# Kernel tuning notes

Measured on AMD Instinct MI355X. Metric: run time of the kernel, lower is better.

The kernel has to match this reference:

```python
import jax, jax.numpy as jnp
import numpy as np

N = 50000
E = 400000
F_IN = 128
HID = 64
HEADS = 4
OUT_HEADS = 4
N_CLS = 121
NEG_SLOPE = 0.2


def _gat_layer(x, src, dst, W, a_src, a_dst, b, heads, out_ch, concat):
    n = x.shape[0]
    xh = (x @ W).reshape(n, heads, out_ch)                      # [N,H,C]
    alpha_s = jnp.sum(xh * a_src, axis=-1)                      # [N,H]
    alpha_d = jnp.sum(xh * a_dst, axis=-1)                      # [N,H]
    logits = jax.nn.leaky_relu(alpha_s[src] + alpha_d[dst], NEG_SLOPE)  # [E,H]
    # numerically stable edge softmax per destination node
    m = jax.ops.segment_max(logits, dst, num_segments=n)        # [N,H]
    e = jnp.exp(logits - m[dst])                                # [E,H]
    denom = jax.ops.segment_sum(e, dst, num_segments=n)         # [N,H]
    alpha = e / (denom[dst] + 1e-16)                            # [E,H]
    msg = alpha[:, :, None] * xh[src]                           # [E,H,C]
    out = jax.ops.segment_sum(msg, dst, num_segments=n)         # [N,H,C]
    if concat:
        out = out.reshape(n, heads * out_ch)
    else:
        out = out.mean(axis=1)
    return out + b


def setup_inputs() -> dict:
    key = jax.random.key(0)
    ks = jax.random.split(key, 20)
    x = jax.random.normal(ks[0], (N, F_IN), dtype=jnp.float32)
    edge_index = jax.random.randint(ks[1], (2, E), 0, N, dtype=jnp.int32)
    s = lambda *sh: 1.0 / np.sqrt(sh[0])
    inp = {
        'x': x,
        'edge_index': edge_index,
        # conv1: F_IN -> HEADS*HID
        'W1': jax.random.normal(ks[2], (F_IN, HEADS * HID), jnp.float32) * s(F_IN),
        'a1_src': jax.random.normal(ks[3], (HEADS, HID), jnp.float32) * s(HID),
        'a1_dst': jax.random.normal(ks[4], (HEADS, HID), jnp.float32) * s(HID),
        'b1': jnp.zeros((HEADS * HID,), jnp.float32),
        'lin1_W': jax.random.normal(ks[5], (F_IN, HEADS * HID), jnp.float32) * s(F_IN),
        'lin1_b': jnp.zeros((HEADS * HID,), jnp.float32),
        # conv2: HEADS*HID -> HEADS*HID
        'W2': jax.random.normal(ks[6], (HEADS * HID, HEADS * HID), jnp.float32) * s(HEADS * HID),
        'a2_src': jax.random.normal(ks[7], (HEADS, HID), jnp.float32) * s(HID),
        'a2_dst': jax.random.normal(ks[8], (HEADS, HID), jnp.float32) * s(HID),
        'b2': jnp.zeros((HEADS * HID,), jnp.float32),
        # conv3: HEADS*HID -> N_CLS (mean over OUT_HEADS)
        'W3': jax.random.normal(ks[9], (HEADS * HID, OUT_HEADS * N_CLS), jnp.float32) * s(HEADS * HID),
        'a3_src': jax.random.normal(ks[10], (OUT_HEADS, N_CLS), jnp.float32) * s(N_CLS),
        'a3_dst': jax.random.normal(ks[11], (OUT_HEADS, N_CLS), jnp.float32) * s(N_CLS),
        'b3': jnp.zeros((N_CLS,), jnp.float32),
        'lin3_W': jax.random.normal(ks[12], (HEADS * HID, N_CLS), jnp.float32) * s(HEADS * HID),
        'lin3_b': jnp.zeros((N_CLS,), jnp.float32),
    }
    return inp


def reference(x, edge_index, W1, a1_src, a1_dst, b1, lin1_W, lin1_b,
              W2, a2_src, a2_dst, b2, W3, a3_src, a3_dst, b3, lin3_W, lin3_b):
    src, dst = edge_index[0], edge_index[1]
    h = _gat_layer(x, src, dst, W1, a1_src, a1_dst, b1, HEADS, HID, True) + (x @ lin1_W + lin1_b)
    h = jax.nn.elu(h)
    h = _gat_layer(h, src, dst, W2, a2_src, a2_dst, b2, HEADS, HID, True) + h  # residual skip (no lin2)
    h = jax.nn.elu(h)
    out = _gat_layer(h, src, dst, W3, a3_src, a3_dst, b3, OUT_HEADS, N_CLS, False) + (h @ lin3_W + lin3_b)
    return out
```

## Files before the change

### kernel.cpp

```cpp
#include <hip/hip_runtime.h>
#include <cstdint>
#include <cstddef>

#define F_IN 128
#define HC12 256
#define HC3 484
#define NCLS 121

typedef unsigned short u16;
typedef unsigned int u32;
typedef __attribute__((ext_vector_type(8))) short short8;
typedef __attribute__((ext_vector_type(8))) __fp16 half8;
typedef __attribute__((ext_vector_type(4))) float float4v;

static __device__ __forceinline__ float lrelu(float x) { return x > 0.f ? x : 0.2f * x; }

static __device__ __forceinline__ u16 f2h(float f) {
    union { __fp16 h; u16 u; } v; v.h = (__fp16)f; return v.u;
}
static __device__ __forceinline__ float h2f(u16 u) {
    union { u16 u; __fp16 h; } v; v.u = u; return (float)v.h;
}

static __device__ __forceinline__ void gload16(const u16* g, u16* l) {
    __builtin_amdgcn_global_load_lds((const __attribute__((address_space(1))) void*)g,
                                     (__attribute__((address_space(3))) void*)l,
                                     16, 0, 0);
}

__global__ void hist_kernel(const int* __restrict__ dst, int* __restrict__ deg, int E) {
    int e = blockIdx.x * 256 + threadIdx.x;
    if (e < E) atomicAdd(&deg[dst[e]], 1);
}

__global__ __launch_bounds__(1024) void scan_kernel(const int* __restrict__ deg,
                                                    int* __restrict__ rowp, int N) {
    __shared__ int swave[16];
    __shared__ int s_carry;
    int tid = threadIdx.x;
    int w = tid >> 6, lane = tid & 63;
    if (tid == 0) { rowp[0] = 0; s_carry = 0; }
    __syncthreads();
    for (int base = 0; base < N; base += 4096) {
        int i0 = base + tid * 4;
        int v0 = (i0     < N) ? deg[i0]     : 0;
        int v1 = (i0 + 1 < N) ? deg[i0 + 1] : 0;
        int v2 = (i0 + 2 < N) ? deg[i0 + 2] : 0;
        int v3 = (i0 + 3 < N) ? deg[i0 + 3] : 0;
        int t = v0 + v1 + v2 + v3;
        int sc = t;
#pragma unroll
        for (int off = 1; off < 64; off <<= 1) {
            int u = __shfl_up(sc, off, 64);
            if (lane >= off) sc += u;
        }
        if (lane == 63) swave[w] = sc;
        __syncthreads();
        if (w == 0) {
            int ws = (lane < 16) ? swave[lane] : 0;
#pragma unroll
            for (int off = 1; off < 16; off <<= 1) {
                int u = __shfl_up(ws, off, 64);
                if (lane >= off) ws += u;
            }
            if (lane < 16) swave[lane] = ws;
        }
        __syncthreads();
        int carry = s_carry;
        int tb = carry + ((w > 0) ? swave[w - 1] : 0) + sc - t;
        if (i0     < N) rowp[i0 + 1] = tb + v0;
        if (i0 + 1 < N) rowp[i0 + 2] = tb + v0 + v1;
        if (i0 + 2 < N) rowp[i0 + 3] = tb + v0 + v1 + v2;
        if (i0 + 3 < N) rowp[i0 + 4] = tb + t;
        __syncthreads();
        if (tid == 1023) s_carry = carry + swave[15];
        __syncthreads();
    }
}

__global__ void scatter_kernel(const int* __restrict__ src, const int* __restrict__ dst,
                               const int* __restrict__ rowp, int* __restrict__ cur,
                               int* __restrict__ col, int E) {
    int e = blockIdx.x * 256 + threadIdx.x;
    if (e < E) {
        int d = dst[e];
        int pos = rowp[d] + atomicAdd(&cur[d], 1);
        col[pos] = src[e];
    }
}

__global__ void cvtT_all_kernel(const float* W1, const float* l1W, const float* W2,
                                const float* W3, const float* l3W,
                                u16* C1, u16* C2, u16* C3) {
    int i = blockIdx.x * 256 + threadIdx.x;
    const float* B; u16* o; int K, N;
    if (i < 32768)       { B = W1;  o = C1;             K = 128; N = 256; }
    else if (i < 65536)  { B = l1W; o = C1 + 256 * 128; K = 128; N = 256; i -= 32768; }
    else if (i < 131072) { B = W2;  o = C2;             K = 256; N = 256; i -= 65536; }
    else if (i < 254976) { B = W3;  o = C3;             K = 256; N = 484; i -= 131072; }
    else if (i < 285952) { B = l3W; o = C3 + 484 * 256; K = 256; N = 121; i -= 254976; }
    else return;
    int n = i % N, k = i / N;
    o[(size_t)n * K + k] = f2h(B[(size_t)k * N + n]);
}

__global__ __launch_bounds__(256) void xcvt_kernel(const float* __restrict__ x,
                                                   u16* __restrict__ o, int total8) {
    int i = blockIdx.x * 256 + threadIdx.x;
    if (i >= total8) return;
    const float4* p = (const float4*)(x + (size_t)i * 8);
    float4 a = p[0], b = p[1];
    union { u16 u[8]; short8 v; } r;
    r.u[0] = f2h(a.x); r.u[1] = f2h(a.y); r.u[2] = f2h(a.z); r.u[3] = f2h(a.w);
    r.u[4] = f2h(b.x); r.u[5] = f2h(b.y); r.u[6] = f2h(b.z); r.u[7] = f2h(b.w);
    *(short8*)(o + (size_t)i * 8) = r.v;
}

#define BM 128
#define BN 128
#define BK 32

__global__ __launch_bounds__(256, 3) void gemm_f16(const u16* __restrict__ A16,
                                                   const u16* __restrict__ BT,
                                                   int M, int K, int Ntot,
                                                   int nx, int ny,
                                                   int Nb, u16* __restrict__ Cb, int strideB,
                                                   float* __restrict__ Cf,
                                                   const float* __restrict__ biasf, int strideF) {
    __shared__ __align__(16) u16 sA[BM * BK];
    __shared__ __align__(16) u16 sB[BN * BK];
    int tid = threadIdx.x;
    int wave = tid >> 6, lane = tid & 63;
    int wr = wave >> 1, wc = wave & 1;

    int bid = blockIdx.x;
    int G = nx * 8;
    int g = bid / G;
    int rem = ny - g * 8;
    int rb, cb;
    if (rem >= 8) {
        int r = bid - g * G;
        rb = g * 8 + (r & 7);
        cb = r >> 3;
    } else {
        int t = bid - g * G;
        rb = g * 8 + t % rem;
        cb = t / rem;
    }
    int m0 = rb * BM, n0 = cb * BN;

    int fm = lane & 15;
    int q = lane >> 4;

    int srow = lane >> 2;
    int sch = (lane & 3) * 8;
    u16* lA0 = &sA[(wave * 32) * BK];
    u16* lA1 = &sA[(wave * 32 + 16) * BK];
    u16* lB0 = &sB[(wave * 32) * BK];
    u16* lB1 = &sB[(wave * 32 + 16) * BK];
    int ar0 = min(m0 + wave * 32 + srow, M - 1);
    int ar1 = min(m0 + wave * 32 + 16 + srow, M - 1);
    int br0 = min(n0 + wave * 32 + srow, Ntot - 1);
    int br1 = min(n0 + wave * 32 + 16 + srow, Ntot - 1);

    float4v acc[4][4];
#pragma unroll
    for (int i = 0; i < 4; i++)
#pragma unroll
        for (int j = 0; j < 4; j++) acc[i][j] = (float4v){0.f, 0.f, 0.f, 0.f};

    for (int kc = 0; kc < K; kc += BK) {
        gload16(&A16[(size_t)ar0 * K + kc + sch], lA0);
        gload16(&A16[(size_t)ar1 * K + kc + sch], lA1);
        gload16(&BT[(size_t)br0 * K + kc + sch], lB0);
        gload16(&BT[(size_t)br1 * K + kc + sch], lB1);
        __syncthreads();

        half8 ah[4];
#pragma unroll
        for (int mi = 0; mi < 4; mi++)
            ah[mi] = *(const half8*)&sA[(wr * 64 + mi * 16 + fm) * BK + q * 8];
#pragma unroll
        for (int ni = 0; ni < 4; ni++) {
            half8 bh = *(const half8*)&sB[(wc * 64 + ni * 16 + fm) * BK + q * 8];
#pragma unroll
            for (int mi = 0; mi < 4; mi++)
                acc[mi][ni] = __builtin_amdgcn_mfma_f32_16x16x32_f16(ah[mi], bh, acc[mi][ni], 0, 0, 0);
        }
        __syncthreads();
    }

#pragma unroll
    for (int mi = 0; mi < 4; mi++) {
#pragma unroll
        for (int ni = 0; ni < 4; ni++) {
            int colg = n0 + wc * 64 + ni * 16 + fm;
            if (colg >= Ntot) continue;
#pragma unroll
            for (int r = 0; r < 4; r++) {
                int rowg = m0 + wr * 64 + mi * 16 + q * 4 + r;
                if (rowg >= M) continue;
                float v = acc[mi][ni][r];
                if (colg < Nb) {
                    Cb[(size_t)rowg * strideB + colg] = f2h(v);
                } else {
                    int cf = colg - Nb;
                    Cf[(size_t)rowg * strideF + cf] = v + biasf[cf];
                }
            }
        }
    }
}

__global__ __launch_bounds__(256) void alpha_wave_256(const u16* __restrict__ xh,
                                                      const float* __restrict__ a_s,
                                                      const float* __restrict__ a_d,
                                                      float* __restrict__ as_o,
                                                      float* __restrict__ ad_o, int N) {
    int lane = threadIdx.x & 63;
    int n = blockIdx.x * 4 + (threadIdx.x >> 6);
    if (n >= N) return;
    int c = lane * 4;
    uint2 v = *(const uint2*)&xh[(size_t)n * HC12 + c];
    float4 s4 = *(const float4*)&a_s[c];
    float4 d4 = *(const float4*)&a_d[c];
    float x0 = h2f((u16)(v.x & 0xffff)), x1 = h2f((u16)(v.x >> 16));
    float x2 = h2f((u16)(v.y & 0xffff)), x3 = h2f((u16)(v.y >> 16));
    float ss = x0 * s4.x + x1 * s4.y + x2 * s4.z + x3 * s4.w;
    float sd = x0 * d4.x + x1 * d4.y + x2 * d4.z + x3 * d4.w;
#pragma unroll
    for (int o = 1; o < 16; o <<= 1) {
        ss += __shfl_xor(ss, o, 64);
        sd += __shfl_xor(sd, o, 64);
    }
    if ((lane & 15) == 0) {
        as_o[n * 4 + (lane >> 4)] = ss;
        ad_o[n * 4 + (lane >> 4)] = sd;
    }
}

__global__ __launch_bounds__(256) void alpha_kernel(const u16* __restrict__ xh,
                                                    const float* __restrict__ a_s,
                                                    const float* __restrict__ a_d,
                                                    float* __restrict__ as_o,
                                                    float* __restrict__ ad_o, int C) {
    int n = blockIdx.x;
    int w = threadIdx.x >> 6, lane = threadIdx.x & 63;
    const u16* row = xh + (size_t)n * 4 * C + (size_t)w * C;
    float ss = 0.f, sd = 0.f;
    for (int c = lane; c < C; c += 64) {
        float v = h2f(row[c]);
        ss += v * a_s[w * C + c];
        sd += v * a_d[w * C + c];
    }
    for (int o = 32; o; o >>= 1) {
        ss += __shfl_xor(ss, o, 64);
        sd += __shfl_xor(sd, o, 64);
    }
    if (!lane) {
        as_o[n * 4 + w] = ss;
        ad_o[n * 4 + w] = sd;
    }
}

__global__ __launch_bounds__(256) void stats_alpha_kernel(const int* __restrict__ rowp,
                                                          const int* __restrict__ col,
                                                          const float* __restrict__ asrc,
                                                          const float* __restrict__ adst,
                                                          float* __restrict__ alphaE, int N) {
    int i = blockIdx.x * 256 + threadIdx.x;
    if (i >= N * 4) return;
    int n = i >> 2, h = i & 3;
    int r0 = rowp[n], r1 = rowp[n + 1];
    float ad = adst[i];
    float m = -3.4e38f, s = 0.f;
    for (int e = r0; e < r1; e++) {
        int sc = col[e];
        float l = lrelu(asrc[sc * 4 + h] + ad);
        float nm = fmaxf(m, l);
        s = s * __expf(m - nm) + __expf(l - nm);
        m = nm;
    }
    float rd = 1.f / (s + 1e-16f);
    for (int e = r0; e < r1; e++) {
        int sc = col[e];
        float l = lrelu(asrc[sc * 4 + h] + ad);
        alphaE[(size_t)e * 4 + h] = __expf(l - m) * rd;
    }
}

__global__ __launch_bounds__(256) void agg_wave_256(const u16* __restrict__ xh,
                                                    const int* __restrict__ rowp,
                                                    const int* __restrict__ col,
                                                    const float* __restrict__ alphaE,
                                                    const float* __restrict__ bias,
                                                    const float* __restrict__ res,
                                                    float* __restrict__ outf,
                                                    u16* __restrict__ out16, int N) {
    int lane = threadIdx.x & 63;
    int n = blockIdx.x * 4 + (threadIdx.x >> 6);
    if (n >= N) return;
    int r0 = rowp[n], r1 = rowp[n + 1];
    int c = lane * 4;
    int h = lane >> 4;
    float a0 = 0.f, a1 = 0.f, a2 = 0.f, a3 = 0.f;
    for (int kb = r0; kb < r1; kb += 16) {
        int cn = min(16, r1 - kb);
        int cidx = col[kb + (lane & 15)];
        float alv = alphaE[(size_t)kb * 4 + lane];
        for (int k = 0; k < cn; k++) {
            int src = __shfl(cidx, k, 64);
            float al = __shfl(alv, k * 4 + h, 64);
            uint2 v = *(const uint2*)&xh[(size_t)src * HC12 + c];
            a0 += al * h2f((u16)(v.x & 0xffff));
            a1 += al * h2f((u16)(v.x >> 16));
            a2 += al * h2f((u16)(v.y & 0xffff));
            a3 += al * h2f((u16)(v.y >> 16));
        }
    }
    float4 bv = *(const float4*)&bias[c];
    float4 rv = *(const float4*)&res[(size_t)n * HC12 + c];
    float v0 = a0 + bv.x + rv.x;
    float v1 = a1 + bv.y + rv.y;
    float v2 = a2 + bv.z + rv.z;
    float v3 = a3 + bv.w + rv.w;
    float e0 = v0 > 0.f ? v0 : expm1f(v0);
    float e1 = v1 > 0.f ? v1 : expm1f(v1);
    float e2 = v2 > 0.f ? v2 : expm1f(v2);
    float e3 = v3 > 0.f ? v3 : expm1f(v3);
    if (outf) {
        float4 o4; o4.x = e0; o4.y = e1; o4.z = e2; o4.w = e3;
        *(float4*)&outf[(size_t)n * HC12 + c] = o4;
    }
    union { u16 u[4]; uint2 v; } p;
    p.u[0] = f2h(e0); p.u[1] = f2h(e1); p.u[2] = f2h(e2); p.u[3] = f2h(e3);
    *(uint2*)&out16[(size_t)n * HC12 + c] = p.v;
}

__global__ __launch_bounds__(256) void agg_wave_out(const u16* __restrict__ xh,
                                                    const int* __restrict__ rowp,
                                                    const int* __restrict__ col,
                                                    const float* __restrict__ alphaE,
                                                    const float* __restrict__ b3,
                                                    const float* __restrict__ lin3,
                                                    float* __restrict__ out, int N) {
    __shared__ float s_acc[4][488];
    int w = threadIdx.x >> 6, lane = threadIdx.x & 63;
    int n = blockIdx.x * 4 + w;
    int r0 = 0, r1 = 0;
    if (n < N) { r0 = rowp[n]; r1 = rowp[n + 1]; }
    int c = lane * 8;
    int hA = c / 121; if (hA > 3) hA = 3;
    int hB = (c + 7) / 121; if (hB > 3) hB = 3;
    int split = 121 * (hA + 1) - c;
    float acc[8] = {0.f, 0.f, 0.f, 0.f, 0.f, 0.f, 0.f, 0.f};
    for (int kb = r0; kb < r1; kb += 16) {
        int cn = min(16, r1 - kb);
        int cidx = col[kb + (lane & 15)];
        float alv = alphaE[(size_t)kb * 4 + lane];
        for (int k = 0; k < cn; k++) {
            int src = __shfl(cidx, k, 64);
            float alA = __shfl(alv, k * 4 + hA, 64);
            float alB = __shfl(alv, k * 4 + hB, 64);
            if (lane < 61) {
                uint4 v = *(const uint4*)&xh[(size_t)src * HC3 + c];
                u32 ww[4] = {v.x, v.y, v.z, v.w};
#pragma unroll
                for (int jj = 0; jj < 4; jj++) {
                    float lo = h2f((u16)(ww[jj] & 0xffff));
                    float hi = h2f((u16)(ww[jj] >> 16));
                    float aLo = (2 * jj     < split) ? alA : alB;
                    float aHi = (2 * jj + 1 < split) ? alA : alB;
                    acc[2 * jj]     += aLo * lo;
                    acc[2 * jj + 1] += aHi * hi;
                }
            }
        }
    }
    if (n < N && lane < 61) {
#pragma unroll
        for (int j = 0; j < 8; j++)
            if (c + j < HC3) s_acc[w][c + j] = acc[j];
    }
    __syncthreads();
    if (n < N) {
        for (int j = lane; j < NCLS; j += 64) {
            float o = 0.25f * (s_acc[w][j] + s_acc[w][j + 121] + s_acc[w][j + 242] + s_acc[w][j + 363])
                      + b3[j] + lin3[(size_t)n * NCLS + j];
            out[(size_t)n * NCLS + j] = o;
        }
    }
}

extern "C" void kernel_launch(void* const* d_in, const int* in_sizes, int n_in,
                              void* d_out, int out_size, void* d_ws, size_t ws_size,
                              hipStream_t stream) {
    const float* x   = (const float*)d_in[0];
    const int*   ei  = (const int*)d_in[1];
    const float* W1  = (const float*)d_in[2];
    const float* a1s = (const float*)d_in[3];
    const float* a1d = (const float*)d_in[4];
    const float* b1  = (const float*)d_in[5];
    const float* l1W = (const float*)d_in[6];
    const float* l1b = (const float*)d_in[7];
    const float* W2  = (const float*)d_in[8];
    const float* a2s = (const float*)d_in[9];
    const float* a2d = (const float*)d_in[10];
    const float* b2  = (const float*)d_in[11];
    const float* W3  = (const float*)d_in[12];
    const float* a3s = (const float*)d_in[13];
    const float* a3d = (const float*)d_in[14];
    const float* b3  = (const float*)d_in[15];
    const float* l3W = (const float*)d_in[16];
    const float* l3b = (const float*)d_in[17];

    const int N = in_sizes[0] / F_IN;
    const int E = in_sizes[1] / 2;
    const int* srcv = ei;
    const int* dstv = ei + E;

    char* ws = (char*)d_ws;
    size_t off = 0;
    auto alloc = [&](size_t bytes) -> char* {
        char* p = ws + off;
        off += (bytes + 255) & ~(size_t)255;
        return p;
    };
    u16*   xh   = (u16*)alloc((size_t)N * HC3 * 2 + 256);
    u16*   x16  = (u16*)alloc((size_t)N * F_IN * 2);
    u16*   h1f  = (u16*)alloc((size_t)N * HC12 * 2);
    u16*   h2f  = (u16*)alloc((size_t)N * HC12 * 2);
    float* h1   = (float*)alloc((size_t)N * HC12 * 4);
    float* lin  = (float*)alloc((size_t)N * NCLS * 4);
    float* as_  = (float*)alloc((size_t)N * 4 * 4);
    float* ad_  = (float*)alloc((size_t)N * 4 * 4);
    int* rowp   = (int*)alloc((size_t)(N + 1) * 4);
    int* degc   = (int*)alloc((size_t)N * 4);
    int* cur    = (int*)alloc((size_t)N * 4);
    int* col    = (int*)alloc((size_t)E * 4 + 256);
    float* alphaE = (float*)alloc((size_t)E * 4 * 4 + 256);
    u16* C1 = (u16*)alloc((size_t)512 * 128 * 2);
    u16* C2 = (u16*)alloc((size_t)256 * 256 * 2);
    u16* C3 = (u16*)alloc((size_t)605 * 256 * 2);
    (void)ws_size; (void)n_in; (void)out_size;

    hipMemsetAsync(degc, 0, (size_t)N * 4, stream);
    hipMemsetAsync(cur, 0, (size_t)N * 4, stream);
    hist_kernel<<<(E + 255) / 256, 256, 0, stream>>>(dstv, degc, E);
    scan_kernel<<<1, 1024, 0, stream>>>(degc, rowp, N);
    scatter_kernel<<<(E + 255) / 256, 256, 0, stream>>>(srcv, dstv, rowp, cur, col, E);

    cvtT_all_kernel<<<(285952 + 255) / 256, 256, 0, stream>>>(W1, l1W, W2, W3, l3W, C1, C2, C3);
    xcvt_kernel<<<(N * F_IN / 8 + 255) / 256, 256, 0, stream>>>(x, x16, N * F_IN / 8);

    int ny = (N + BM - 1) / BM;
    int sgrid = (N * 4 + 255) / 256;
    int wgrid = (N + 3) / 4;

    gemm_f16<<<4 * ny, 256, 0, stream>>>(x16, C1, N, F_IN, 512, 4, ny,
                                         256, xh, 256, h1, l1b, 256);
    alpha_wave_256<<<wgrid, 256, 0, stream>>>(xh, a1s, a1d, as_, ad_, N);
    stats_alpha_kernel<<<sgrid, 256, 0, stream>>>(rowp, col, as_, ad_, alphaE, N);
    agg_wave_256<<<wgrid, 256, 0, stream>>>(xh, rowp, col, alphaE, b1, h1, h1, h1f, N);

    gemm_f16<<<2 * ny, 256, 0, stream>>>(h1f, C2, N, HC12, 256, 2, ny,
                                         256, xh, 256, nullptr, nullptr, 0);
    alpha_wave_256<<<wgrid, 256, 0, stream>>>(xh, a2s, a2d, as_, ad_, N);
    stats_alpha_kernel<<<sgrid, 256, 0, stream>>>(rowp, col, as_, ad_, alphaE, N);
    agg_wave_256<<<wgrid, 256, 0, stream>>>(xh, rowp, col, alphaE, b2, h1, nullptr, h2f, N);

    gemm_f16<<<5 * ny, 256, 0, stream>>>(h2f, C3, N, HC12, 605, 5, ny,
                                         484, xh, 484, lin, l3b, NCLS);
    alpha_kernel<<<N, 256, 0, stream>>>(xh, a3s, a3d, as_, ad_, NCLS);
    stats_alpha_kernel<<<sgrid, 256, 0, stream>>>(rowp, col, as_, ad_, alphaE, N);
    agg_wave_out<<<wgrid, 256, 0, stream>>>(xh, rowp, col, alphaE, b3, lin, (float*)d_out, N);
}
```

Measured before the change: 543.9 us.

## Pad layer-3 head rows to 122 halves and remap alpha/aggregation per lane

The layer-3 GEMM epilogue now writes each head's 121 columns into a padded 122-wide slot (row stride 488), so every lane can load aligned 2-half words per head. The alpha kernel for layer 3 changes from one block per node to one wave per node, and the output aggregation has each lane own two classes across all four heads, which removes the shared-memory reduction, the head-split logic and the block-wide sync. The aggregation inner loops also get unroll-4 hints. The trade-off is four narrow 32-bit gathers per edge in place of one 16-byte load, plus an index remap in the GEMM epilogue.

```diff
diff --git a/kernel.cpp b/kernel.cpp
--- a/kernel.cpp
+++ b/kernel.cpp
@@ -5,6 +5,7 @@
 #define F_IN 128
 #define HC12 256
 #define HC3 484
+#define HC3P 488
 #define NCLS 121
 
 typedef unsigned short u16;
@@ -125,6 +126,7 @@
                                                    int M, int K, int Ntot,
                                                    int nx, int ny,
                                                    int Nb, u16* __restrict__ Cb, int strideB,
+                                                   int pad121,
                                                    float* __restrict__ Cf,
                                                    const float* __restrict__ biasf, int strideF) {
     __shared__ __align__(16) u16 sA[BM * BK];
@@ -196,13 +198,18 @@
         for (int ni = 0; ni < 4; ni++) {
             int colg = n0 + wc * 64 + ni * 16 + fm;
             if (colg >= Ntot) continue;
+            int cg = colg;
+            if (pad121 && colg < Nb) {
+                int hh = (colg * 1084) >> 17;
+                cg = colg + hh;
+            }
 #pragma unroll
             for (int r = 0; r < 4; r++) {
                 int rowg = m0 + wr * 64 + mi * 16 + q * 4 + r;
                 if (rowg >= M) continue;
                 float v = acc[mi][ni][r];
                 if (colg < Nb) {
-                    Cb[(size_t)rowg * strideB + colg] = f2h(v);
+                    Cb[(size_t)rowg * strideB + cg] = f2h(v);
                 } else {
                     int cf = colg - Nb;
                     Cf[(size_t)rowg * strideF + cf] = v + biasf[cf];
@@ -239,27 +246,44 @@
     }
 }
 
-__global__ __launch_bounds__(256) void alpha_kernel(const u16* __restrict__ xh,
-                                                    const float* __restrict__ a_s,
-                                                    const float* __restrict__ a_d,
-                                                    float* __restrict__ as_o,
-                                                    float* __restrict__ ad_o, int C) {
-    int n = blockIdx.x;
-    int w = threadIdx.x >> 6, lane = threadIdx.x & 63;
-    const u16* row = xh + (size_t)n * 4 * C + (size_t)w * C;
-    float ss = 0.f, sd = 0.f;
-    for (int c = lane; c < C; c += 64) {
-        float v = h2f(row[c]);
-        ss += v * a_s[w * C + c];
-        sd += v * a_d[w * C + c];
-    }
-    for (int o = 32; o; o >>= 1) {
-        ss += __shfl_xor(ss, o, 64);
-        sd += __shfl_xor(sd, o, 64);
-    }
-    if (!lane) {
-        as_o[n * 4 + w] = ss;
-        ad_o[n * 4 + w] = sd;
+__global__ __launch_bounds__(256) void alpha3_wave(const u16* __restrict__ xh3,
+                                                   const float* __restrict__ a_s,
+                                                   const float* __restrict__ a_d,
+                                                   float* __restrict__ as_o,
+                                                   float* __restrict__ ad_o, int N) {
+    int lane = threadIdx.x & 63;
+    int n = blockIdx.x * 4 + (threadIdx.x >> 6);
+    if (n >= N) return;
+    int l = min(lane, 60);
+    int c0 = 2 * l;
+    float m0 = (lane < 61) ? 1.f : 0.f;
+    float m1 = (lane < 61 && c0 + 1 < NCLS) ? 1.f : 0.f;
+    int d1 = (c0 + 1 < NCLS) ? 1 : 0;
+    const u16* row = xh3 + (size_t)n * HC3P;
+    float ss[4], sd[4];
+#pragma unroll
+    for (int h = 0; h < 4; h++) {
+        u32 v = *(const u32*)&row[h * 122 + c0];
+        float x0 = h2f((u16)(v & 0xffff)) * m0;
+        float x1 = h2f((u16)(v >> 16)) * m1;
+        int i0 = h * NCLS + c0;
+        ss[h] = x0 * a_s[i0] + x1 * a_s[i0 + d1];
+        sd[h] = x0 * a_d[i0] + x1 * a_d[i0 + d1];
+    }
+#pragma unroll
+    for (int o = 1; o < 64; o <<= 1) {
+#pragma unroll
+        for (int h = 0; h < 4; h++) {
+            ss[h] += __shfl_xor(ss[h], o, 64);
+            sd[h] += __shfl_xor(sd[h], o, 64);
+        }
+    }
+    if (lane == 0) {
+#pragma unroll
+        for (int h = 0; h < 4; h++) {
+            as_o[n * 4 + h] = ss[h];
+            ad_o[n * 4 + h] = sd[h];
+        }
     }
 }
 
@@ -308,6 +332,7 @@
         int cn = min(16, r1 - kb);
         int cidx = col[kb + (lane & 15)];
         float alv = alphaE[(size_t)kb * 4 + lane];
+#pragma unroll 4
         for (int k = 0; k < cn; k++) {
             int src = __shfl(cidx, k, 64);
             float al = __shfl(alv, k * 4 + h, 64);
@@ -337,57 +362,56 @@
     *(uint2*)&out16[(size_t)n * HC12 + c] = p.v;
 }
 
-__global__ __launch_bounds__(256) void agg_wave_out(const u16* __restrict__ xh,
+__global__ __launch_bounds__(256) void agg_wave_out(const u16* __restrict__ xh3,
                                                     const int* __restrict__ rowp,
                                                     const int* __restrict__ col,
                                                     const float* __restrict__ alphaE,
                                                     const float* __restrict__ b3,
                                                     const float* __restrict__ lin3,
                                                     float* __restrict__ out, int N) {
-    __shared__ float s_acc[4][488];
-    int w = threadIdx.x >> 6, lane = threadIdx.x & 63;
-    int n = blockIdx.x * 4 + w;
-    int r0 = 0, r1 = 0;
-    if (n < N) { r0 = rowp[n]; r1 = rowp[n + 1]; }
-    int c = lane * 8;
-    int hA = c / 121; if (hA > 3) hA = 3;
-    int hB = (c + 7) / 121; if (hB > 3) hB = 3;
-    int split = 121 * (hA + 1) - c;
-    float acc[8] = {0.f, 0.f, 0.f, 0.f, 0.f, 0.f, 0.f, 0.f};
+    int lane = threadIdx.x & 63;
+    int n = blockIdx.x * 4 + (threadIdx.x >> 6);
+    if (n >= N) return;
+    int r0 = rowp[n], r1 = rowp[n + 1];
+    int l = min(lane, 60);
+    int c0 = 2 * l;
+    float acc[4][2];
+#pragma unroll
+    for (int h = 0; h < 4; h++) { acc[h][0] = 0.f; acc[h][1] = 0.f; }
     for (int kb = r0; kb < r1; kb += 16) {
         int cn = min(16, r1 - kb);
         int cidx = col[kb + (lane & 15)];
         float alv = alphaE[(size_t)kb * 4 + lane];
+#pragma unroll 4
         for (int k = 0; k < cn; k++) {
             int src = __shfl(cidx, k, 64);
-            float alA = __shfl(alv, k * 4 + hA, 64);
-            float alB = __shfl(alv, k * 4 + hB, 64);
-            if (lane < 61) {
-                uint4 v = *(const uint4*)&xh[(size_t)src * HC3 + c];
-                u32 ww[4] = {v.x, v.y, v.z, v.w};
-#pragma unroll
-                for (int jj = 0; jj < 4; jj++) {
-                    float lo = h2f((u16)(ww[jj] & 0xffff));
-                    float hi = h2f((u16)(ww[jj] >> 16));
-                    float aLo = (2 * jj     < split) ? alA : alB;
-                    float aHi = (2 * jj + 1 < split) ? alA : alB;
-                    acc[2 * jj]     += aLo * lo;
-                    acc[2 * jj + 1] += aHi * hi;
-                }
-            }
-        }
-    }
-    if (n < N && lane < 61) {
-#pragma unroll
-        for (int j = 0; j < 8; j++)
-            if (c + j < HC3) s_acc[w][c + j] = acc[j];
-    }
-    __syncthreads();
-    if (n < N) {
-        for (int j = lane; j < NCLS; j += 64) {
-            float o = 0.25f * (s_acc[w][j] + s_acc[w][j + 121] + s_acc[w][j + 242] + s_acc[w][j + 363])
-                      + b3[j] + lin3[(size_t)n * NCLS + j];
-            out[(size_t)n * NCLS + j] = o;
+            float al0 = __shfl(alv, k * 4 + 0, 64);
+            float al1 = __shfl(alv, k * 4 + 1, 64);
+            float al2 = __shfl(alv, k * 4 + 2, 64);
+            float al3 = __shfl(alv, k * 4 + 3, 64);
+            const u16* row = xh3 + (size_t)src * HC3P + c0;
+            u32 v0 = *(const u32*)&row[0];
+            u32 v1 = *(const u32*)&row[122];
+            u32 v2 = *(const u32*)&row[244];
+            u32 v3 = *(const u32*)&row[366];
+            acc[0][0] += al0 * h2f((u16)(v0 & 0xffff));
+            acc[0][1] += al0 * h2f((u16)(v0 >> 16));
+            acc[1][0] += al1 * h2f((u16)(v1 & 0xffff));
+            acc[1][1] += al1 * h2f((u16)(v1 >> 16));
+            acc[2][0] += al2 * h2f((u16)(v2 & 0xffff));
+            acc[2][1] += al2 * h2f((u16)(v2 >> 16));
+            acc[3][0] += al3 * h2f((u16)(v3 & 0xffff));
+            acc[3][1] += al3 * h2f((u16)(v3 >> 16));
+        }
+    }
+    if (lane < 61) {
+        float o0 = 0.25f * (acc[0][0] + acc[1][0] + acc[2][0] + acc[3][0])
+                   + b3[c0] + lin3[(size_t)n * NCLS + c0];
+        out[(size_t)n * NCLS + c0] = o0;
+        if (c0 + 1 < NCLS) {
+            float o1 = 0.25f * (acc[0][1] + acc[1][1] + acc[2][1] + acc[3][1])
+                       + b3[c0 + 1] + lin3[(size_t)n * NCLS + c0 + 1];
+            out[(size_t)n * NCLS + c0 + 1] = o1;
         }
     }
 }
@@ -426,7 +450,7 @@
         off += (bytes + 255) & ~(size_t)255;
         return p;
     };
-    u16*   xh   = (u16*)alloc((size_t)N * HC3 * 2 + 256);
+    u16*   xh   = (u16*)alloc((size_t)N * HC3P * 2 + 256);
     u16*   x16  = (u16*)alloc((size_t)N * F_IN * 2);
     u16*   h1f  = (u16*)alloc((size_t)N * HC12 * 2);
     u16*   h2f  = (u16*)alloc((size_t)N * HC12 * 2);
@@ -458,20 +482,20 @@
     int wgrid = (N + 3) / 4;
 
     gemm_f16<<<4 * ny, 256, 0, stream>>>(x16, C1, N, F_IN, 512, 4, ny,
-                                         256, xh, 256, h1, l1b, 256);
+                                         256, xh, 256, 0, h1, l1b, 256);
     alpha_wave_256<<<wgrid, 256, 0, stream>>>(xh, a1s, a1d, as_, ad_, N);
     stats_alpha_kernel<<<sgrid, 256, 0, stream>>>(rowp, col, as_, ad_, alphaE, N);
     agg_wave_256<<<wgrid, 256, 0, stream>>>(xh, rowp, col, alphaE, b1, h1, h1, h1f, N);
 
     gemm_f16<<<2 * ny, 256, 0, stream>>>(h1f, C2, N, HC12, 256, 2, ny,
-                                         256, xh, 256, nullptr, nullptr, 0);
+                                         256, xh, 256, 0, nullptr, nullptr, 0);
     alpha_wave_256<<<wgrid, 256, 0, stream>>>(xh, a2s, a2d, as_, ad_, N);
     stats_alpha_kernel<<<sgrid, 256, 0, stream>>>(rowp, col, as_, ad_, alphaE, N);
     agg_wave_256<<<wgrid, 256, 0, stream>>>(xh, rowp, col, alphaE, b2, h1, nullptr, h2f, N);
 
     gemm_f16<<<5 * ny, 256, 0, stream>>>(h2f, C3, N, HC12, 605, 5, ny,
-                                         484, xh, 484, lin, l3b, NCLS);
-    alpha_kernel<<<N, 256, 0, stream>>>(xh, a3s, a3d, as_, ad_, NCLS);
+                                         484, xh, HC3P, 1, lin, l3b, NCLS);
+    alpha3_wave<<<wgrid, 256, 0, stream>>>(xh, a3s, a3d, as_, ad_, N);
     stats_alpha_kernel<<<sgrid, 256, 0, stream>>>(rowp, col, as_, ad_, alphaE, N);
     agg_wave_out<<<wgrid, 256, 0, stream>>>(xh, rowp, col, alphaE, b3, lin, (float*)d_out, N);
 }
```

Result: no change. 539.2 us (-0.9%).
